# Performance work log

Measured on AMD Instinct MI355X. Metric: run time of the kernel, lower is better.

## Reference

```python
import jax, jax.numpy as jnp
import numpy as np

N_DAYS, N_HOURS, N_LINKS, N_FEATS = 4, 24, 2000, 4
N_PATHS, N_ODS = 20000, 4000
EPS = 1e-12


def setup_inputs() -> dict:
    key = jax.random.key(0)
    ks = jax.random.split(key, 9)
    # X: (days, hours, links, 1 + n_features); channel 0 is free-flow travel time tt_ff
    X = jax.random.uniform(ks[0], (N_DAYS, N_HOURS, N_LINKS, N_FEATS + 1), dtype=jnp.float32) + 0.1
    # utility coefficients; signs '-' for all cost features (projected via clip to <= 0)
    theta_raw = -jax.random.uniform(ks[1], (N_FEATS,), dtype=jnp.float32)
    theta_links = 0.01 * jax.random.normal(ks[2], (N_LINKS,), dtype=jnp.float32)
    q_sqrt = jax.random.uniform(ks[3], (N_ODS,), dtype=jnp.float32) + 0.5  # q = q_sqrt**2
    log_alpha = 0.1 * jax.random.normal(ks[4], (N_LINKS,), dtype=jnp.float32)
    beta_raw = jax.random.uniform(ks[5], (N_LINKS,), dtype=jnp.float32, minval=1.0, maxval=3.0)
    k = jax.random.uniform(ks[6], (N_LINKS,), dtype=jnp.float32, minval=50.0, maxval=150.0)
    # link-path incidence D (n_links, n_paths), ~10 links per path
    D = (jax.random.uniform(ks[7], (N_LINKS, N_PATHS)) < 0.005).astype(jnp.float32)
    # OD segment id of each path (sorted, one OD per path) == sparse M structure
    od_of_path = jnp.sort(jax.random.randint(ks[8], (N_PATHS,), 0, N_ODS, dtype=jnp.int32))
    return dict(X=X, theta_raw=theta_raw, theta_links=theta_links, q_sqrt=q_sqrt,
                log_alpha=log_alpha, beta_raw=beta_raw, k=k, D=D,
                od_of_path=od_of_path, n_ods=N_ODS)


def reference(X, theta_raw, theta_links, q_sqrt, log_alpha, beta_raw, k, D, od_of_path, n_ods):
    # project_theta: all features have sign '-', so clip to (-inf, 0]
    theta = jnp.minimum(theta_raw, 0.0)
    tt_ff = X[..., 0]              # (d, h, l)
    feats = X[..., 1:]             # (d, h, l, f)
    # link utilities: einsum('ijkl,l->ijk') + theta_links
    V = jnp.einsum('dhlf,f->dhl', feats, theta) + theta_links
    # path utilities: einsum('ijk,kl->ijl') with D (links, paths)
    vf = jnp.einsum('dhl,lp->dhp', V, D)            # (d, h, p)
    vf_t = jnp.moveaxis(vf, -1, 0)                  # (p, d, h) paths leading for segment ops
    # segmented softmax over paths within each OD choice set (sparse M pattern)
    vmax = jax.lax.stop_gradient(
        jax.ops.segment_max(vf_t, od_of_path, num_segments=n_ods))   # (ods, d, h)
    ev = jnp.exp(vf_t - vmax[od_of_path])
    denom = jax.ops.segment_sum(ev, od_of_path, num_segments=n_ods)[od_of_path]
    pf = ev / denom                                  # (p, d, h) path probabilities
    # path flows: pf scaled by OD demand q = q_sqrt**2
    q = q_sqrt ** 2
    f = pf * q[od_of_path][:, None, None]            # (p, d, h)
    # link flows + relu
    x = jax.nn.relu(jnp.einsum('pdh,lp->dhl', f, D))  # (d, h, l)
    # BPR link travel times: tt_ff * (1 + alpha * (x/k)^beta)
    alpha = jnp.exp(log_alpha)
    beta = jnp.clip(beta_raw, EPS, 4.0)
    return tt_ff * (1.0 + alpha * jnp.power(x / k, beta))
```

## Files before the change

### kernel.cpp

```cpp
#include <hip/hip_runtime.h>
#include <math.h>

#define NDH 96
#define ND4 24
#define NL  2000
#define NP  20000
#define NOD 4000
#define PL_CAP 32
#define LP_CAP 150
#define LP_LDS 256

typedef unsigned short u16;
typedef unsigned int   u32;
typedef u32 v4u __attribute__((ext_vector_type(4)));

__device__ __forceinline__ int lower_bound_od(const int* __restrict__ od, int key) {
    int lo = 0, hi = NP;
    while (lo < hi) { int mid = (lo + hi) >> 1; if (od[mid] < key) lo = mid + 1; else hi = mid; }
    return lo;
}

__global__ __launch_bounds__(256) void kBV(const float* __restrict__ D,
                                           const float* __restrict__ X,
                                           const float* __restrict__ theta_raw,
                                           const float* __restrict__ theta_links,
                                           const int* __restrict__ od,
                                           float* __restrict__ V,
                                           int* __restrict__ start,
                                           int* __restrict__ lc,
                                           u16* __restrict__ lp,
                                           int* __restrict__ pc,
                                           u16* __restrict__ pl) {
    __shared__ u16 slp[LP_LDS];
    __shared__ int scnt;
    int l = blockIdx.x;
    int tid = threadIdx.x;
    if (tid == 0) scnt = 0;

    if (tid < NDH) {
        float t0 = fminf(theta_raw[0], 0.f);
        float t1 = fminf(theta_raw[1], 0.f);
        float t2 = fminf(theta_raw[2], 0.f);
        float t3 = fminf(theta_raw[3], 0.f);
        const float* xp = X + ((size_t)(tid * NL + l)) * 5;
        V[l * NDH + tid] = theta_links[l]
                         + t0 * xp[1] + t1 * xp[2] + t2 * xp[3] + t3 * xp[4];
    } else if (tid < 98) {
        int sid = l * 2 + (tid - 96);
        start[sid] = lower_bound_od(od, sid);
    } else if (tid == 98 && l == 0) {
        start[NOD] = lower_bound_od(od, NOD);
    }
    __syncthreads();

    const v4u* row4 = (const v4u*)(D + (size_t)l * NP);
    for (int base = 0; base < 5000; base += 2048) {
        v4u v[8];
        int idx[8];
#pragma unroll
        for (int k = 0; k < 8; k++) {
            idx[k] = base + k * 256 + tid;
            if (idx[k] < 5000) {
                v[k] = __builtin_nontemporal_load(row4 + idx[k]);
            } else {
                v[k][0] = 0u; v[k][1] = 0u; v[k][2] = 0u; v[k][3] = 0u;
            }
        }
#pragma unroll
        for (int k = 0; k < 8; k++) {
            if ((v[k][0] | v[k][1] | v[k][2] | v[k][3]) == 0u) continue;
            int p0 = idx[k] * 4;
            if (v[k][0]) { int s = atomicAdd(&scnt, 1); if (s < LP_LDS) slp[s] = (u16)(p0);     }
            if (v[k][1]) { int s = atomicAdd(&scnt, 1); if (s < LP_LDS) slp[s] = (u16)(p0 + 1); }
            if (v[k][2]) { int s = atomicAdd(&scnt, 1); if (s < LP_LDS) slp[s] = (u16)(p0 + 2); }
            if (v[k][3]) { int s = atomicAdd(&scnt, 1); if (s < LP_LDS) slp[s] = (u16)(p0 + 3); }
        }
    }
    __syncthreads();
    int c = min(scnt, LP_CAP);
    for (int j = tid; j < c; j += 256) {
        int p = (int)slp[j];
        lp[l * LP_CAP + j] = (u16)p;
        int s = atomicAdd(&pc[p], 1);
        if (s < PL_CAP) pl[p * PL_CAP + s] = (u16)l;
    }
    if (tid == 0) lc[l] = scnt;
}

__global__ __launch_bounds__(256) void kD4(const float* __restrict__ V,
                                           const int* __restrict__ pc,
                                           const u16* __restrict__ pl,
                                           float* __restrict__ vf) {
    int tid = blockIdx.x * blockDim.x + threadIdx.x;
    if (tid >= NP * ND4) return;
    int p = tid / ND4, d4 = tid - p * ND4;
    int c = min(pc[p], PL_CAP);
    const u16* plrow = pl + p * PL_CAP;
    const float4* V4 = (const float4*)V;
    float4 acc = make_float4(0.f, 0.f, 0.f, 0.f);
    for (int j0 = 0; j0 < c; j0 += 8) {
        int li[8];
#pragma unroll
        for (int t = 0; t < 8; t++) li[t] = (j0 + t < c) ? (int)plrow[j0 + t] : -1;
#pragma unroll
        for (int t = 0; t < 8; t++) {
            if (li[t] >= 0) {
                float4 v = V4[li[t] * ND4 + d4];
                acc.x += v.x; acc.y += v.y; acc.z += v.z; acc.w += v.w;
            }
        }
    }
    ((float4*)vf)[p * ND4 + d4] = acc;
}

__global__ __launch_bounds__(256) void kE4(float* __restrict__ vf,
                                           const int* __restrict__ start,
                                           const float* __restrict__ q_sqrt) {
    int tid = blockIdx.x * blockDim.x + threadIdx.x;
    if (tid >= NOD * ND4) return;
    int o = tid / ND4, d4 = tid - o * ND4;
    int a = start[o], b = start[o + 1];
    if (a >= b) return;
    float4* vf4 = (float4*)vf;
    float4 m = make_float4(-INFINITY, -INFINITY, -INFINITY, -INFINITY);
    for (int p = a; p < b; p++) {
        float4 v = vf4[p * ND4 + d4];
        m.x = fmaxf(m.x, v.x); m.y = fmaxf(m.y, v.y);
        m.z = fmaxf(m.z, v.z); m.w = fmaxf(m.w, v.w);
    }
    float4 s = make_float4(0.f, 0.f, 0.f, 0.f);
    for (int p = a; p < b; p++) {
        float4 v = vf4[p * ND4 + d4];
        s.x += expf(v.x - m.x); s.y += expf(v.y - m.y);
        s.z += expf(v.z - m.z); s.w += expf(v.w - m.w);
    }
    float q = q_sqrt[o]; float qq = q * q;
    float4 rs = make_float4(qq / s.x, qq / s.y, qq / s.z, qq / s.w);
    for (int p = a; p < b; p++) {
        float4 v = vf4[p * ND4 + d4];
        v.x = expf(v.x - m.x) * rs.x; v.y = expf(v.y - m.y) * rs.y;
        v.z = expf(v.z - m.z) * rs.z; v.w = expf(v.w - m.w) * rs.w;
        vf4[p * ND4 + d4] = v;
    }
}

__global__ __launch_bounds__(192) void kF4(const float* __restrict__ f,
                                           const int* __restrict__ lc,
                                           const u16* __restrict__ lp,
                                           const float* __restrict__ X,
                                           const float* __restrict__ log_alpha,
                                           const float* __restrict__ beta_raw,
                                           const float* __restrict__ kk,
                                           float* __restrict__ out) {
    __shared__ float4 sf[8 * ND4];
    __shared__ u16 slp2[LP_CAP];
    int l  = blockIdx.x;
    int c  = min(lc[l], LP_CAP);
    for (int j = threadIdx.x; j < c; j += 192) slp2[j] = lp[l * LP_CAP + j];
    __syncthreads();
    int d4 = threadIdx.x % ND4;
    int jc = threadIdx.x / ND4;
    const float4* f4 = (const float4*)f;
    float4 acc = make_float4(0.f, 0.f, 0.f, 0.f);
    for (int j0 = jc; j0 < c; j0 += 32) {
        int jj[4];
#pragma unroll
        for (int t = 0; t < 4; t++) {
            int j = j0 + t * 8;
            jj[t] = (j < c) ? (int)slp2[j] : -1;
        }
#pragma unroll
        for (int t = 0; t < 4; t++) {
            if (jj[t] >= 0) {
                float4 v = f4[jj[t] * ND4 + d4];
                acc.x += v.x; acc.y += v.y; acc.z += v.z; acc.w += v.w;
            }
        }
    }
    sf[jc * ND4 + d4] = acc;
    __syncthreads();
    if (jc == 0) {
        float4 t = sf[d4];
#pragma unroll
        for (int r = 1; r < 8; r++) {
            float4 u = sf[r * ND4 + d4];
            t.x += u.x; t.y += u.y; t.z += u.z; t.w += u.w;
        }
        float alpha = expf(log_alpha[l]);
        float beta  = fminf(fmaxf(beta_raw[l], 1e-12f), 4.0f);
        float kv    = kk[l];
        float xs[4] = { t.x, t.y, t.z, t.w };
#pragma unroll
        for (int k4 = 0; k4 < 4; k4++) {
            int dh = d4 * 4 + k4;
            float xv = fmaxf(xs[k4], 0.f);
            float tt = X[((size_t)(dh * NL + l)) * 5];
            out[dh * NL + l] = tt * (1.0f + alpha * powf(xv / kv, beta));
        }
    }
}

extern "C" void kernel_launch(void* const* d_in, const int* in_sizes, int n_in,
                              void* d_out, int out_size, void* d_ws, size_t ws_size,
                              hipStream_t stream) {
    const float* X           = (const float*)d_in[0];
    const float* theta_raw   = (const float*)d_in[1];
    const float* theta_links = (const float*)d_in[2];
    const float* q_sqrt      = (const float*)d_in[3];
    const float* log_alpha   = (const float*)d_in[4];
    const float* beta_raw    = (const float*)d_in[5];
    const float* kk          = (const float*)d_in[6];
    const float* D           = (const float*)d_in[7];
    const int*   od          = (const int*)d_in[8];
    float* out = (float*)d_out;
    char* ws = (char*)d_ws;

    int*   pc    = (int*)(ws + 0);
    int*   lc    = (int*)(ws + 80000);
    int*   start = (int*)(ws + 88064);
    float* V     = (float*)(ws + 104576);
    u16*   pl    = (u16*)(ws + 872576);
    u16*   lp    = (u16*)(ws + 2152576);
    float* vf    = (float*)(ws + 2785024);

    hipMemsetAsync(pc, 0, 80000, stream);

    kBV <<<NL, 256, 0, stream>>>(D, X, theta_raw, theta_links, od, V, start, lc, lp, pc, pl);
    kD4 <<<(NP * ND4 + 255) / 256, 256, 0, stream>>>(V, pc, pl, vf);
    kE4 <<<(NOD * ND4 + 255) / 256, 256, 0, stream>>>(vf, start, q_sqrt);
    kF4 <<<NL, 192, 0, stream>>>(vf, lc, lp, X, log_alpha, beta_raw, kk, out);
}
```

Measured before the change: 283.8 us.

## Fuse all stages into one persistent kernel with grid-wide barriers

Replaces the memset and four separate kernel launches with a single persistent kernel of 512 blocks. Stages are separated by a software global barrier built on an atomic counter. The pc zeroing moves into the kernel, and the softmax now stores exp values in its second pass so the third pass does not recompute them. This removes launch gaps and the memset. In exchange the D-scan and link-gather stages get far fewer blocks than before (2000 down to 512), and correctness depends on all blocks being co-resident for the spin barrier.

Result: slower. 583.2 us (+105.5%).

```diff
diff --git a/kernel.cpp b/kernel.cpp
--- a/kernel.cpp
+++ b/kernel.cpp
@@ -9,6 +9,8 @@
 #define PL_CAP 32
 #define LP_CAP 150
 #define LP_LDS 256
+#define GRID 512
+#define TPB  256
 
 typedef unsigned short u16;
 typedef unsigned int   u32;
@@ -20,182 +22,199 @@
     return lo;
 }
 
-__global__ __launch_bounds__(256) void kBV(const float* __restrict__ D,
-                                           const float* __restrict__ X,
-                                           const float* __restrict__ theta_raw,
-                                           const float* __restrict__ theta_links,
-                                           const int* __restrict__ od,
-                                           float* __restrict__ V,
-                                           int* __restrict__ start,
-                                           int* __restrict__ lc,
-                                           u16* __restrict__ lp,
-                                           int* __restrict__ pc,
-                                           u16* __restrict__ pl) {
+__device__ __forceinline__ void gbar(int* cnt, int phase) {
+    __syncthreads();
+    if (threadIdx.x == 0) {
+        __hip_atomic_fetch_add(cnt, 1, __ATOMIC_ACQ_REL, __HIP_MEMORY_SCOPE_AGENT);
+        const int target = phase * GRID;
+        while (__hip_atomic_load(cnt, __ATOMIC_ACQUIRE, __HIP_MEMORY_SCOPE_AGENT) < target) {
+            __builtin_amdgcn_s_sleep(2);
+        }
+    }
+    __syncthreads();
+}
+
+__global__ __launch_bounds__(TPB, 2) void mega(
+        const float* __restrict__ X,
+        const float* __restrict__ theta_raw,
+        const float* __restrict__ theta_links,
+        const float* __restrict__ q_sqrt,
+        const float* __restrict__ log_alpha,
+        const float* __restrict__ beta_raw,
+        const float* __restrict__ kk,
+        const float* __restrict__ D,
+        const int*   __restrict__ od,
+        float* __restrict__ out,
+        int* __restrict__ pc, int* __restrict__ lc, int* __restrict__ start,
+        float* __restrict__ V, u16* __restrict__ pl, u16* __restrict__ lp,
+        float* __restrict__ vf, int* __restrict__ barcnt) {
     __shared__ u16 slp[LP_LDS];
     __shared__ int scnt;
-    int l = blockIdx.x;
-    int tid = threadIdx.x;
-    if (tid == 0) scnt = 0;
-
-    if (tid < NDH) {
+    __shared__ float4 sf[10 * ND4];
+    __shared__ u16 slp2[LP_CAP + 2];
+
+    const int tid  = threadIdx.x;
+    const int gtid = blockIdx.x * TPB + tid;
+    const int gstr = GRID * TPB;
+
+    for (int i = gtid; i < NP; i += gstr) pc[i] = 0;
+    for (int i = gtid; i <= NOD; i += gstr) start[i] = lower_bound_od(od, i);
+    {
         float t0 = fminf(theta_raw[0], 0.f);
         float t1 = fminf(theta_raw[1], 0.f);
         float t2 = fminf(theta_raw[2], 0.f);
         float t3 = fminf(theta_raw[3], 0.f);
-        const float* xp = X + ((size_t)(tid * NL + l)) * 5;
-        V[l * NDH + tid] = theta_links[l]
-                         + t0 * xp[1] + t1 * xp[2] + t2 * xp[3] + t3 * xp[4];
-    } else if (tid < 98) {
-        int sid = l * 2 + (tid - 96);
-        start[sid] = lower_bound_od(od, sid);
-    } else if (tid == 98 && l == 0) {
-        start[NOD] = lower_bound_od(od, NOD);
-    }
-    __syncthreads();
-
-    const v4u* row4 = (const v4u*)(D + (size_t)l * NP);
-    for (int base = 0; base < 5000; base += 2048) {
-        v4u v[8];
-        int idx[8];
-#pragma unroll
-        for (int k = 0; k < 8; k++) {
-            idx[k] = base + k * 256 + tid;
-            if (idx[k] < 5000) {
-                v[k] = __builtin_nontemporal_load(row4 + idx[k]);
-            } else {
-                v[k][0] = 0u; v[k][1] = 0u; v[k][2] = 0u; v[k][3] = 0u;
-            }
-        }
-#pragma unroll
-        for (int k = 0; k < 8; k++) {
-            if ((v[k][0] | v[k][1] | v[k][2] | v[k][3]) == 0u) continue;
-            int p0 = idx[k] * 4;
-            if (v[k][0]) { int s = atomicAdd(&scnt, 1); if (s < LP_LDS) slp[s] = (u16)(p0);     }
-            if (v[k][1]) { int s = atomicAdd(&scnt, 1); if (s < LP_LDS) slp[s] = (u16)(p0 + 1); }
-            if (v[k][2]) { int s = atomicAdd(&scnt, 1); if (s < LP_LDS) slp[s] = (u16)(p0 + 2); }
-            if (v[k][3]) { int s = atomicAdd(&scnt, 1); if (s < LP_LDS) slp[s] = (u16)(p0 + 3); }
-        }
-    }
-    __syncthreads();
-    int c = min(scnt, LP_CAP);
-    for (int j = tid; j < c; j += 256) {
-        int p = (int)slp[j];
-        lp[l * LP_CAP + j] = (u16)p;
-        int s = atomicAdd(&pc[p], 1);
-        if (s < PL_CAP) pl[p * PL_CAP + s] = (u16)l;
-    }
-    if (tid == 0) lc[l] = scnt;
-}
-
-__global__ __launch_bounds__(256) void kD4(const float* __restrict__ V,
-                                           const int* __restrict__ pc,
-                                           const u16* __restrict__ pl,
-                                           float* __restrict__ vf) {
-    int tid = blockIdx.x * blockDim.x + threadIdx.x;
-    if (tid >= NP * ND4) return;
-    int p = tid / ND4, d4 = tid - p * ND4;
-    int c = min(pc[p], PL_CAP);
-    const u16* plrow = pl + p * PL_CAP;
-    const float4* V4 = (const float4*)V;
-    float4 acc = make_float4(0.f, 0.f, 0.f, 0.f);
-    for (int j0 = 0; j0 < c; j0 += 8) {
-        int li[8];
-#pragma unroll
-        for (int t = 0; t < 8; t++) li[t] = (j0 + t < c) ? (int)plrow[j0 + t] : -1;
-#pragma unroll
-        for (int t = 0; t < 8; t++) {
-            if (li[t] >= 0) {
-                float4 v = V4[li[t] * ND4 + d4];
-                acc.x += v.x; acc.y += v.y; acc.z += v.z; acc.w += v.w;
-            }
-        }
-    }
-    ((float4*)vf)[p * ND4 + d4] = acc;
-}
-
-__global__ __launch_bounds__(256) void kE4(float* __restrict__ vf,
-                                           const int* __restrict__ start,
-                                           const float* __restrict__ q_sqrt) {
-    int tid = blockIdx.x * blockDim.x + threadIdx.x;
-    if (tid >= NOD * ND4) return;
-    int o = tid / ND4, d4 = tid - o * ND4;
-    int a = start[o], b = start[o + 1];
-    if (a >= b) return;
-    float4* vf4 = (float4*)vf;
-    float4 m = make_float4(-INFINITY, -INFINITY, -INFINITY, -INFINITY);
-    for (int p = a; p < b; p++) {
-        float4 v = vf4[p * ND4 + d4];
-        m.x = fmaxf(m.x, v.x); m.y = fmaxf(m.y, v.y);
-        m.z = fmaxf(m.z, v.z); m.w = fmaxf(m.w, v.w);
-    }
-    float4 s = make_float4(0.f, 0.f, 0.f, 0.f);
-    for (int p = a; p < b; p++) {
-        float4 v = vf4[p * ND4 + d4];
-        s.x += expf(v.x - m.x); s.y += expf(v.y - m.y);
-        s.z += expf(v.z - m.z); s.w += expf(v.w - m.w);
-    }
-    float q = q_sqrt[o]; float qq = q * q;
-    float4 rs = make_float4(qq / s.x, qq / s.y, qq / s.z, qq / s.w);
-    for (int p = a; p < b; p++) {
-        float4 v = vf4[p * ND4 + d4];
-        v.x = expf(v.x - m.x) * rs.x; v.y = expf(v.y - m.y) * rs.y;
-        v.z = expf(v.z - m.z) * rs.z; v.w = expf(v.w - m.w) * rs.w;
-        vf4[p * ND4 + d4] = v;
-    }
-}
-
-__global__ __launch_bounds__(192) void kF4(const float* __restrict__ f,
-                                           const int* __restrict__ lc,
-                                           const u16* __restrict__ lp,
-                                           const float* __restrict__ X,
-                                           const float* __restrict__ log_alpha,
-                                           const float* __restrict__ beta_raw,
-                                           const float* __restrict__ kk,
-                                           float* __restrict__ out) {
-    __shared__ float4 sf[8 * ND4];
-    __shared__ u16 slp2[LP_CAP];
-    int l  = blockIdx.x;
-    int c  = min(lc[l], LP_CAP);
-    for (int j = threadIdx.x; j < c; j += 192) slp2[j] = lp[l * LP_CAP + j];
-    __syncthreads();
-    int d4 = threadIdx.x % ND4;
-    int jc = threadIdx.x / ND4;
-    const float4* f4 = (const float4*)f;
-    float4 acc = make_float4(0.f, 0.f, 0.f, 0.f);
-    for (int j0 = jc; j0 < c; j0 += 32) {
-        int jj[4];
-#pragma unroll
-        for (int t = 0; t < 4; t++) {
-            int j = j0 + t * 8;
-            jj[t] = (j < c) ? (int)slp2[j] : -1;
-        }
-#pragma unroll
-        for (int t = 0; t < 4; t++) {
-            if (jj[t] >= 0) {
-                float4 v = f4[jj[t] * ND4 + d4];
-                acc.x += v.x; acc.y += v.y; acc.z += v.z; acc.w += v.w;
-            }
-        }
-    }
-    sf[jc * ND4 + d4] = acc;
-    __syncthreads();
-    if (jc == 0) {
-        float4 t = sf[d4];
-#pragma unroll
-        for (int r = 1; r < 8; r++) {
-            float4 u = sf[r * ND4 + d4];
-            t.x += u.x; t.y += u.y; t.z += u.z; t.w += u.w;
-        }
-        float alpha = expf(log_alpha[l]);
-        float beta  = fminf(fmaxf(beta_raw[l], 1e-12f), 4.0f);
-        float kv    = kk[l];
-        float xs[4] = { t.x, t.y, t.z, t.w };
-#pragma unroll
-        for (int k4 = 0; k4 < 4; k4++) {
-            int dh = d4 * 4 + k4;
-            float xv = fmaxf(xs[k4], 0.f);
-            float tt = X[((size_t)(dh * NL + l)) * 5];
-            out[dh * NL + l] = tt * (1.0f + alpha * powf(xv / kv, beta));
+        for (int g = gtid; g < NL * NDH; g += gstr) {
+            int l = g / NDH, dh = g - l * NDH;
+            const float* xp = X + ((size_t)(dh * NL + l)) * 5;
+            V[g] = theta_links[l] + t0 * xp[1] + t1 * xp[2] + t2 * xp[3] + t3 * xp[4];
+        }
+    }
+    gbar(barcnt, 1);
+
+    for (int l = blockIdx.x; l < NL; l += GRID) {
+        if (tid == 0) scnt = 0;
+        __syncthreads();
+        const v4u* row4 = (const v4u*)(D + (size_t)l * NP);
+        for (int base = 0; base < 5000; base += 2048) {
+            v4u v[8];
+            int idx[8];
+#pragma unroll
+            for (int k = 0; k < 8; k++) {
+                idx[k] = base + k * 256 + tid;
+                if (idx[k] < 5000) {
+                    v[k] = __builtin_nontemporal_load(row4 + idx[k]);
+                } else {
+                    v[k][0] = 0u; v[k][1] = 0u; v[k][2] = 0u; v[k][3] = 0u;
+                }
+            }
+#pragma unroll
+            for (int k = 0; k < 8; k++) {
+                if ((v[k][0] | v[k][1] | v[k][2] | v[k][3]) == 0u) continue;
+                int p0 = idx[k] * 4;
+                if (v[k][0]) { int s = atomicAdd(&scnt, 1); if (s < LP_LDS) slp[s] = (u16)(p0);     }
+                if (v[k][1]) { int s = atomicAdd(&scnt, 1); if (s < LP_LDS) slp[s] = (u16)(p0 + 1); }
+                if (v[k][2]) { int s = atomicAdd(&scnt, 1); if (s < LP_LDS) slp[s] = (u16)(p0 + 2); }
+                if (v[k][3]) { int s = atomicAdd(&scnt, 1); if (s < LP_LDS) slp[s] = (u16)(p0 + 3); }
+            }
+        }
+        __syncthreads();
+        int c = min(scnt, LP_CAP);
+        for (int j = tid; j < c; j += TPB) {
+            int p = (int)slp[j];
+            lp[l * LP_CAP + j] = (u16)p;
+            int s = atomicAdd(&pc[p], 1);
+            if (s < PL_CAP) pl[p * PL_CAP + s] = (u16)l;
+        }
+        if (tid == 0) lc[l] = scnt;
+        __syncthreads();
+    }
+    gbar(barcnt, 2);
+
+    {
+        const float4* V4 = (const float4*)V;
+        for (int t = gtid; t < NP * ND4; t += gstr) {
+            int p = t / ND4, d4 = t - p * ND4;
+            int c = min(pc[p], PL_CAP);
+            const u16* plrow = pl + p * PL_CAP;
+            float4 acc = make_float4(0.f, 0.f, 0.f, 0.f);
+            for (int j0 = 0; j0 < c; j0 += 8) {
+                int li[8];
+#pragma unroll
+                for (int q = 0; q < 8; q++) li[q] = (j0 + q < c) ? (int)plrow[j0 + q] : -1;
+#pragma unroll
+                for (int q = 0; q < 8; q++) {
+                    if (li[q] >= 0) {
+                        float4 v = V4[li[q] * ND4 + d4];
+                        acc.x += v.x; acc.y += v.y; acc.z += v.z; acc.w += v.w;
+                    }
+                }
+            }
+            ((float4*)vf)[p * ND4 + d4] = acc;
+        }
+    }
+    gbar(barcnt, 3);
+
+    {
+        float4* vf4 = (float4*)vf;
+        for (int t = gtid; t < NOD * ND4; t += gstr) {
+            int o = t / ND4, d4 = t - o * ND4;
+            int a = start[o], b = start[o + 1];
+            if (a >= b) continue;
+            float4 m = make_float4(-INFINITY, -INFINITY, -INFINITY, -INFINITY);
+            for (int p = a; p < b; p++) {
+                float4 v = vf4[p * ND4 + d4];
+                m.x = fmaxf(m.x, v.x); m.y = fmaxf(m.y, v.y);
+                m.z = fmaxf(m.z, v.z); m.w = fmaxf(m.w, v.w);
+            }
+            float4 s = make_float4(0.f, 0.f, 0.f, 0.f);
+            for (int p = a; p < b; p++) {
+                float4 v = vf4[p * ND4 + d4];
+                float4 e;
+                e.x = expf(v.x - m.x); e.y = expf(v.y - m.y);
+                e.z = expf(v.z - m.z); e.w = expf(v.w - m.w);
+                s.x += e.x; s.y += e.y; s.z += e.z; s.w += e.w;
+                vf4[p * ND4 + d4] = e;
+            }
+            float q = q_sqrt[o]; float qq = q * q;
+            float4 rs = make_float4(qq / s.x, qq / s.y, qq / s.z, qq / s.w);
+            for (int p = a; p < b; p++) {
+                float4 v = vf4[p * ND4 + d4];
+                v.x *= rs.x; v.y *= rs.y; v.z *= rs.z; v.w *= rs.w;
+                vf4[p * ND4 + d4] = v;
+            }
+        }
+    }
+    gbar(barcnt, 4);
+
+    {
+        const float4* f4 = (const float4*)vf;
+        int d4 = tid % ND4;
+        int jc = tid / ND4;
+        for (int l = blockIdx.x; l < NL; l += GRID) {
+            int c = min(lc[l], LP_CAP);
+            for (int j = tid; j < c; j += TPB) slp2[j] = lp[l * LP_CAP + j];
+            __syncthreads();
+            if (jc < 10) {
+                float4 acc = make_float4(0.f, 0.f, 0.f, 0.f);
+                for (int j0 = jc; j0 < c; j0 += 40) {
+                    int jj[4];
+#pragma unroll
+                    for (int q = 0; q < 4; q++) {
+                        int j = j0 + q * 10;
+                        jj[q] = (j < c) ? (int)slp2[j] : -1;
+                    }
+#pragma unroll
+                    for (int q = 0; q < 4; q++) {
+                        if (jj[q] >= 0) {
+                            float4 v = f4[jj[q] * ND4 + d4];
+                            acc.x += v.x; acc.y += v.y; acc.z += v.z; acc.w += v.w;
+                        }
+                    }
+                }
+                sf[jc * ND4 + d4] = acc;
+            }
+            __syncthreads();
+            if (jc == 0) {
+                float4 t = sf[d4];
+#pragma unroll
+                for (int r = 1; r < 10; r++) {
+                    float4 u = sf[r * ND4 + d4];
+                    t.x += u.x; t.y += u.y; t.z += u.z; t.w += u.w;
+                }
+                float alpha = expf(log_alpha[l]);
+                float beta  = fminf(fmaxf(beta_raw[l], 1e-12f), 4.0f);
+                float kv    = kk[l];
+                float xs[4] = { t.x, t.y, t.z, t.w };
+#pragma unroll
+                for (int k4 = 0; k4 < 4; k4++) {
+                    int dh = d4 * 4 + k4;
+                    float xv = fmaxf(xs[k4], 0.f);
+                    float tt = X[((size_t)(dh * NL + l)) * 5];
+                    out[dh * NL + l] = tt * (1.0f + alpha * powf(xv / kv, beta));
+                }
+            }
+            __syncthreads();
         }
     }
 }
@@ -222,11 +241,11 @@
     u16*   pl    = (u16*)(ws + 872576);
     u16*   lp    = (u16*)(ws + 2152576);
     float* vf    = (float*)(ws + 2785024);
-
-    hipMemsetAsync(pc, 0, 80000, stream);
-
-    kBV <<<NL, 256, 0, stream>>>(D, X, theta_raw, theta_links, od, V, start, lc, lp, pc, pl);
-    kD4 <<<(NP * ND4 + 255) / 256, 256, 0, stream>>>(V, pc, pl, vf);
-    kE4 <<<(NOD * ND4 + 255) / 256, 256, 0, stream>>>(vf, start, q_sqrt);
-    kF4 <<<NL, 192, 0, stream>>>(vf, lc, lp, X, log_alpha, beta_raw, kk, out);
-}
+    int*   barcnt= (int*)(ws + 10465280);
+
+    hipMemsetAsync(barcnt, 0, 256, stream);
+
+    mega<<<GRID, TPB, 0, stream>>>(X, theta_raw, theta_links, q_sqrt, log_alpha,
+                                   beta_raw, kk, D, od, out,
+                                   pc, lc, start, V, pl, lp, vf, barcnt);
+}
```
